# Kernel optimization log

Measured on AMD Instinct MI355X. Metric: run time of the kernel, lower is better.

Reference implementation:

```python
import jax, jax.numpy as jnp
import numpy as np

B, N, R, VR = 4, 10475, 48, 96


def setup_inputs() -> dict:
    key = jax.random.key(0)
    k1, k2, k3, k4 = jax.random.split(key, 4)
    v1s = jax.random.normal(k1, (B, N, 3), dtype=jnp.float32)
    v2s = jax.random.normal(k2, (B, N, 3), dtype=jnp.float32)
    cmaps = jax.random.randint(k3, (B, R, R), 0, 2).astype(bool)
    rid_to_vid = jax.random.randint(k4, (R, VR), 0, N, dtype=jnp.int32)
    return {"v1s": v1s, "v2s": v2s, "cmaps": cmaps, "rid_to_vid": rid_to_vid}


def reference(v1s, v2s, cmaps, rid_to_vid):
    # Gather region vertex subsets for ALL regions at once: [B, R, Vr, 3]
    g1 = v1s[:, rid_to_vid, :]
    g2 = v2s[:, rid_to_vid, :]
    # Squared norms per point
    sq1 = jnp.sum(g1 * g1, axis=-1)                 # [B, R, Vr]
    sq2 = jnp.sum(g2 * g2, axis=-1)                 # [B, R, Vr]
    # Inner products for every (region r of person1, region s of person2) pair
    inner = jnp.einsum('brvc,bswc->brsvw', g1, g2)  # [B, R, R, Vr, Vr]
    d2 = sq1[:, :, None, :, None] + sq2[:, None, :, None, :] - 2.0 * inner
    d = jnp.sqrt(jnp.maximum(d2, 0.0))              # squared=False -> euclidean
    # min over the two vertex-subset axes -> per region-pair min distance [B, R, R]
    min_d = jnp.min(d, axis=(3, 4))
    # Original averages min dists only over active contact pairs (torch.where(cmap))
    m = cmaps.astype(min_d.dtype)                   # [B, R, R]
    return jnp.sum(min_d * m, axis=(1, 2)) / jnp.sum(m, axis=(1, 2))
```

## Files before the change

kernel.cpp:

```cpp
#include <hip/hip_runtime.h>

#define B_ 4
#define R_ 48
#define VR_ 96
#define NBLK (B_ * R_ * 12)

typedef float v2f __attribute__((ext_vector_type(2)));
struct F3 { float x, y, z; };

__device__ __forceinline__ int detect_stride4(const unsigned char* cm, int lane) {
  const unsigned int d = ((const unsigned int*)cm)[lane];
  const unsigned int b1 = (d >> 8) & 0xff, b2 = (d >> 16) & 0xff, b3 = d >> 24;
  const unsigned long long nzm = __ballot((b1 | b2 | b3) != 0);
  const unsigned long long bigm = __ballot((b1 > 1) || (b2 > 1) || (b3 > 1));
  return (bigm != 0ull || nzm == 0ull) ? 1 : 0;
}

__global__ __launch_bounds__(256) void fused_cell_kernel(
    const float* __restrict__ v1s, const float* __restrict__ v2s,
    const int* __restrict__ rid_to_vid, const unsigned char* __restrict__ cm,
    float* __restrict__ minbuf, int N) {
  const int bid = blockIdx.x;
  const int b = bid / (R_ * 12);
  const int rem = bid % (R_ * 12);
  const int r = rem / 12;
  const int quad = rem % 12;
  const int t = threadIdx.x;
  const int w = t >> 6, lane = t & 63;
  const int s = quad * 4 + w;
  const int cellIdx = (b * R_ + r) * R_ + s;
  const size_t bN3 = (size_t)b * N * 3;

  F3 pt1;
  const bool have1 = (t < VR_);
  if (have1) {
    const int idx = rid_to_vid[r * VR_ + t];
    pt1 = *(const F3*)(v1s + bN3 + (size_t)idx * 3);
  }
  const int row0 = t / VR_, v0 = t % VR_;
  const int idx0 = rid_to_vid[(quad * 4 + row0) * VR_ + v0];
  const F3 pt2a = *(const F3*)(v2s + bN3 + (size_t)idx0 * 3);
  const int p1 = t + 256;
  const bool have2b = (p1 < 4 * VR_);
  int row1 = 3, v1 = 0;
  F3 pt2b;
  if (have2b) {
    row1 = p1 / VR_; v1 = p1 % VR_;
    const int idx1 = rid_to_vid[(quad * 4 + row1) * VR_ + v1];
    pt2b = *(const F3*)(v2s + bN3 + (size_t)idx1 * 3);
  }

  const int stride4 = detect_stride4(cm, lane);
  const bool active = stride4 ? (((const unsigned int*)cm)[cellIdx] != 0u)
                              : (cm[cellIdx] != 0);

  __shared__ float s1[3 * VR_];
  __shared__ float s2[4][3 * VR_];
  if (have1) { s1[t] = pt1.x; s1[VR_ + t] = pt1.y; s1[2 * VR_ + t] = pt1.z; }
  s2[row0][v0] = pt2a.x; s2[row0][VR_ + v0] = pt2a.y; s2[row0][2 * VR_ + v0] = pt2a.z;
  if (have2b) { s2[row1][v1] = pt2b.x; s2[row1][VR_ + v1] = pt2b.y; s2[row1][2 * VR_ + v1] = pt2b.z; }
  __syncthreads();

  if (!active) return;

  const float* r2 = s2[w];
  const int hi = lane >> 3, lo = lane & 7;

  float Ax[12], Ay[12], Az[12];
  v2f Bx[6], By[6], Bz[6];
#pragma unroll
  for (int k = 0; k < 3; ++k) {
    *(float4*)&Ax[4 * k] = *(const float4*)(s1           + hi * 12 + 4 * k);
    *(float4*)&Ay[4 * k] = *(const float4*)(s1 +     VR_ + hi * 12 + 4 * k);
    *(float4*)&Az[4 * k] = *(const float4*)(s1 + 2 * VR_ + hi * 12 + 4 * k);
    *(float4*)&Bx[2 * k] = *(const float4*)(r2           + lo * 12 + 4 * k);
    *(float4*)&By[2 * k] = *(const float4*)(r2 +     VR_ + lo * 12 + 4 * k);
    *(float4*)&Bz[2 * k] = *(const float4*)(r2 + 2 * VR_ + lo * 12 + 4 * k);
  }

  float acc[4] = {3.4e38f, 3.4e38f, 3.4e38f, 3.4e38f};
#pragma unroll
  for (int i = 0; i < 12; ++i) {
    const v2f axx = {Ax[i], Ax[i]};
    const v2f ayy = {Ay[i], Ay[i]};
    const v2f azz = {Az[i], Az[i]};
#pragma unroll
    for (int j = 0; j < 6; ++j) {
      const v2f dx = axx - Bx[j];
      const v2f dy = ayy - By[j];
      const v2f dz = azz - Bz[j];
      const v2f d2 = dx * dx + dy * dy + dz * dz;
      acc[j & 3] = fminf(acc[j & 3], fminf(d2.x, d2.y));
    }
  }
  float mind2 = fminf(fminf(acc[0], acc[1]), fminf(acc[2], acc[3]));
#pragma unroll
  for (int off = 32; off > 0; off >>= 1)
    mind2 = fminf(mind2, __shfl_down(mind2, off, 64));
  if (lane == 0) minbuf[cellIdx] = sqrtf(fmaxf(mind2, 0.0f));
}

__global__ __launch_bounds__(256) void finalize_kernel(
    const float* __restrict__ min_d, const unsigned char* __restrict__ cm,
    float* __restrict__ out) {
  const int b = blockIdx.x;
  const int t = threadIdx.x;
  const int lane = t & 63;

  const int stride4 = detect_stride4(cm, lane);
  const unsigned int* cm32 = (const unsigned int*)cm;

  float sum = 0.0f, cnt = 0.0f;
  for (int i = t; i < R_ * R_; i += 256) {
    const int gi = b * R_ * R_ + i;
    const bool m = stride4 ? (cm32[gi] != 0u) : (cm[gi] != 0);
    if (m) { sum += min_d[gi]; cnt += 1.0f; }
  }
#pragma unroll
  for (int off = 32; off > 0; off >>= 1) {
    sum += __shfl_down(sum, off, 64);
    cnt += __shfl_down(cnt, off, 64);
  }
  __shared__ float ws_[4], wc_[4];
  if ((t & 63) == 0) { ws_[t >> 6] = sum; wc_[t >> 6] = cnt; }
  __syncthreads();
  if (t == 0) {
    out[b] = (ws_[0] + ws_[1] + ws_[2] + ws_[3]) /
             (wc_[0] + wc_[1] + wc_[2] + wc_[3]);
  }
}

extern "C" void kernel_launch(void* const* d_in, const int* in_sizes, int n_in,
                              void* d_out, int out_size, void* d_ws, size_t ws_size,
                              hipStream_t stream) {
  const float* v1s = (const float*)d_in[0];
  const float* v2s = (const float*)d_in[1];
  const unsigned char* cmaps = (const unsigned char*)d_in[2];
  const int* rid_to_vid = (const int*)d_in[3];
  float* out = (float*)d_out;
  float* minbuf = (float*)d_ws;

  const int N = in_sizes[0] / (B_ * 3);

  fused_cell_kernel<<<NBLK, 256, 0, stream>>>(
      v1s, v2s, rid_to_vid, cmaps, minbuf, N);
  finalize_kernel<<<B_, 256, 0, stream>>>(minbuf, cmaps, out);
}
```

Measured before the change: 23.39 us.

## Fuse finalize into main kernel via atomic partial sums and last-block reduction

Removes the separate finalize kernel. Each block now atomically adds its partial sum of per-cell min distances into padded per-batch slots. A two-level atomic counter (groups of 64 blocks, then a master counter) picks the last block, which reads the slots, counts the active mask entries and writes the per-batch means. This saves one kernel launch and the minbuf round trip, but adds a hipMemsetAsync of the control buffer, global atomics in every block, and serial mask counting in one final block.

```diff
diff --git a/kernel.cpp b/kernel.cpp
--- a/kernel.cpp
+++ b/kernel.cpp
@@ -4,9 +4,12 @@
 #define R_ 48
 #define VR_ 96
 #define NBLK (B_ * R_ * 12)
+#define NGRP 36
+#define SLOTS_PER_B 16
 
 typedef float v2f __attribute__((ext_vector_type(2)));
 struct F3 { float x, y, z; };
+
 
 __device__ __forceinline__ int detect_stride4(const unsigned char* cm, int lane) {
   const unsigned int d = ((const unsigned int*)cm)[lane];
@@ -16,10 +19,10 @@
   return (bigm != 0ull || nzm == 0ull) ? 1 : 0;
 }
 
-__global__ __launch_bounds__(256) void fused_cell_kernel(
+__global__ __launch_bounds__(256) void fused_all_kernel(
     const float* __restrict__ v1s, const float* __restrict__ v2s,
     const int* __restrict__ rid_to_vid, const unsigned char* __restrict__ cm,
-    float* __restrict__ minbuf, int N) {
+    float* __restrict__ ctrl, float* __restrict__ out, int N) {
   const int bid = blockIdx.x;
   const int b = bid / (R_ * 12);
   const int rem = bid % (R_ * 12);
@@ -30,6 +33,10 @@
   const int s = quad * 4 + w;
   const int cellIdx = (b * R_ + r) * R_ + s;
   const size_t bN3 = (size_t)b * N * 3;
+
+  float* const psum = ctrl;
+  unsigned* const gc = (unsigned*)(ctrl + 1024);
+  unsigned* const master = (unsigned*)(ctrl + 1600);
 
   F3 pt1;
   const bool have1 = (t < VR_);
@@ -51,8 +58,8 @@
   }
 
   const int stride4 = detect_stride4(cm, lane);
-  const bool active = stride4 ? (((const unsigned int*)cm)[cellIdx] != 0u)
-                              : (cm[cellIdx] != 0);
+  const unsigned int* cm32 = (const unsigned int*)cm;
+  const bool active = stride4 ? (cm32[cellIdx] != 0u) : (cm[cellIdx] != 0);
 
   __shared__ float s1[3 * VR_];
   __shared__ float s2[4][3 * VR_];
@@ -61,73 +68,88 @@
   if (have2b) { s2[row1][v1] = pt2b.x; s2[row1][VR_ + v1] = pt2b.y; s2[row1][2 * VR_ + v1] = pt2b.z; }
   __syncthreads();
 
-  if (!active) return;
+  float mind = 0.0f;
+  if (active) {
+    const float* r2 = s2[w];
+    const int hi = lane >> 3, lo = lane & 7;
 
-  const float* r2 = s2[w];
-  const int hi = lane >> 3, lo = lane & 7;
+    float Ax[12], Ay[12], Az[12];
+    v2f Bx[6], By[6], Bz[6];
+#pragma unroll
+    for (int k = 0; k < 3; ++k) {
+      *(float4*)&Ax[4 * k] = *(const float4*)(s1           + hi * 12 + 4 * k);
+      *(float4*)&Ay[4 * k] = *(const float4*)(s1 +     VR_ + hi * 12 + 4 * k);
+      *(float4*)&Az[4 * k] = *(const float4*)(s1 + 2 * VR_ + hi * 12 + 4 * k);
+      *(float4*)&Bx[2 * k] = *(const float4*)(r2           + lo * 12 + 4 * k);
+      *(float4*)&By[2 * k] = *(const float4*)(r2 +     VR_ + lo * 12 + 4 * k);
+      *(float4*)&Bz[2 * k] = *(const float4*)(r2 + 2 * VR_ + lo * 12 + 4 * k);
+    }
 
-  float Ax[12], Ay[12], Az[12];
-  v2f Bx[6], By[6], Bz[6];
+    float acc[4] = {3.4e38f, 3.4e38f, 3.4e38f, 3.4e38f};
 #pragma unroll
-  for (int k = 0; k < 3; ++k) {
-    *(float4*)&Ax[4 * k] = *(const float4*)(s1           + hi * 12 + 4 * k);
-    *(float4*)&Ay[4 * k] = *(const float4*)(s1 +     VR_ + hi * 12 + 4 * k);
-    *(float4*)&Az[4 * k] = *(const float4*)(s1 + 2 * VR_ + hi * 12 + 4 * k);
-    *(float4*)&Bx[2 * k] = *(const float4*)(r2           + lo * 12 + 4 * k);
-    *(float4*)&By[2 * k] = *(const float4*)(r2 +     VR_ + lo * 12 + 4 * k);
-    *(float4*)&Bz[2 * k] = *(const float4*)(r2 + 2 * VR_ + lo * 12 + 4 * k);
+    for (int i = 0; i < 12; ++i) {
+      const v2f axx = {Ax[i], Ax[i]};
+      const v2f ayy = {Ay[i], Ay[i]};
+      const v2f azz = {Az[i], Az[i]};
+#pragma unroll
+      for (int j = 0; j < 6; ++j) {
+        const v2f dx = axx - Bx[j];
+        const v2f dy = ayy - By[j];
+        const v2f dz = azz - Bz[j];
+        const v2f d2 = dx * dx + dy * dy + dz * dz;
+        acc[j & 3] = fminf(acc[j & 3], fminf(d2.x, d2.y));
+      }
+    }
+    float mind2 = fminf(fminf(acc[0], acc[1]), fminf(acc[2], acc[3]));
+#pragma unroll
+    for (int off = 32; off > 0; off >>= 1)
+      mind2 = fminf(mind2, __shfl_down(mind2, off, 64));
+    mind = sqrtf(fmaxf(mind2, 0.0f));
   }
 
-  float acc[4] = {3.4e38f, 3.4e38f, 3.4e38f, 3.4e38f};
-#pragma unroll
-  for (int i = 0; i < 12; ++i) {
-    const v2f axx = {Ax[i], Ax[i]};
-    const v2f ayy = {Ay[i], Ay[i]};
-    const v2f azz = {Az[i], Az[i]};
-#pragma unroll
-    for (int j = 0; j < 6; ++j) {
-      const v2f dx = axx - Bx[j];
-      const v2f dy = ayy - By[j];
-      const v2f dz = azz - Bz[j];
-      const v2f d2 = dx * dx + dy * dy + dz * dz;
-      acc[j & 3] = fminf(acc[j & 3], fminf(d2.x, d2.y));
+  __shared__ float sm[4];
+  __shared__ int finflag;
+  if (t == 0) finflag = 0;
+  if (lane == 0) sm[w] = mind;
+  __syncthreads();
+  if (t == 0) {
+    const float partial = sm[0] + sm[1] + sm[2] + sm[3];
+    atomicAdd(&psum[(b * SLOTS_PER_B + (bid & (SLOTS_PER_B - 1))) * 16], partial);
+    __threadfence();
+    const unsigned old = atomicAdd(&gc[(bid >> 6) * 16], 1u);
+    if (old == 63u) {
+      const unsigned m = atomicAdd(master, 1u);
+      if (m == NGRP - 1u) finflag = 1;
     }
   }
-  float mind2 = fminf(fminf(acc[0], acc[1]), fminf(acc[2], acc[3]));
+  __syncthreads();
+  if (!finflag) return;
+
+  __threadfence();
+  float slotv = 0.0f;
+  if (t < 64) slotv = atomicAdd(&psum[t * 16], 0.0f);
 #pragma unroll
-  for (int off = 32; off > 0; off >>= 1)
-    mind2 = fminf(mind2, __shfl_down(mind2, off, 64));
-  if (lane == 0) minbuf[cellIdx] = sqrtf(fmaxf(mind2, 0.0f));
-}
+  for (int off = 8; off > 0; off >>= 1)
+    slotv += __shfl_down(slotv, off, 16);
+  __shared__ float bsum[4];
+  if (t < 64 && (t & 15) == 0) bsum[t >> 4] = slotv;
 
-__global__ __launch_bounds__(256) void finalize_kernel(
-    const float* __restrict__ min_d, const unsigned char* __restrict__ cm,
-    float* __restrict__ out) {
-  const int b = blockIdx.x;
-  const int t = threadIdx.x;
-  const int lane = t & 63;
-
-  const int stride4 = detect_stride4(cm, lane);
-  const unsigned int* cm32 = (const unsigned int*)cm;
-
-  float sum = 0.0f, cnt = 0.0f;
-  for (int i = t; i < R_ * R_; i += 256) {
-    const int gi = b * R_ * R_ + i;
-    const bool m = stride4 ? (cm32[gi] != 0u) : (cm[gi] != 0);
-    if (m) { sum += min_d[gi]; cnt += 1.0f; }
+  __shared__ float bcnt[4];
+  __shared__ float wc[4];
+  for (int bb = 0; bb < B_; ++bb) {
+    float c = 0.0f;
+    for (int i = t; i < R_ * R_; i += 256) {
+      const int gi = bb * R_ * R_ + i;
+      c += (stride4 ? (cm32[gi] != 0u) : (cm[gi] != 0)) ? 1.0f : 0.0f;
+    }
+#pragma unroll
+    for (int off = 32; off > 0; off >>= 1) c += __shfl_down(c, off, 64);
+    if ((t & 63) == 0) wc[t >> 6] = c;
+    __syncthreads();
+    if (t == 0) bcnt[bb] = wc[0] + wc[1] + wc[2] + wc[3];
+    __syncthreads();
   }
-#pragma unroll
-  for (int off = 32; off > 0; off >>= 1) {
-    sum += __shfl_down(sum, off, 64);
-    cnt += __shfl_down(cnt, off, 64);
-  }
-  __shared__ float ws_[4], wc_[4];
-  if ((t & 63) == 0) { ws_[t >> 6] = sum; wc_[t >> 6] = cnt; }
-  __syncthreads();
-  if (t == 0) {
-    out[b] = (ws_[0] + ws_[1] + ws_[2] + ws_[3]) /
-             (wc_[0] + wc_[1] + wc_[2] + wc_[3]);
-  }
+  if (t < 4) out[t] = bsum[t] / bcnt[t];
 }
 
 extern "C" void kernel_launch(void* const* d_in, const int* in_sizes, int n_in,
@@ -138,11 +160,11 @@
   const unsigned char* cmaps = (const unsigned char*)d_in[2];
   const int* rid_to_vid = (const int*)d_in[3];
   float* out = (float*)d_out;
-  float* minbuf = (float*)d_ws;
+  float* ctrl = (float*)d_ws;
 
   const int N = in_sizes[0] / (B_ * 3);
 
-  fused_cell_kernel<<<NBLK, 256, 0, stream>>>(
-      v1s, v2s, rid_to_vid, cmaps, minbuf, N);
-  finalize_kernel<<<B_, 256, 0, stream>>>(minbuf, cmaps, out);
+  hipMemsetAsync(d_ws, 0, 8192, stream);
+  fused_all_kernel<<<NBLK, 256, 0, stream>>>(
+      v1s, v2s, rid_to_vid, cmaps, ctrl, out, N);
 }
```

Result: slower. 57.78 us (+147.0%).
